# Performance work log

Measured on AMD Instinct MI355X. Metric: run time of the kernel, lower is better.

Reference implementation:

```python
import jax, jax.numpy as jnp
import numpy as np

N_NODES = 32000   # total nodes
NUM_GRAPHS = 32   # B
NODES_PER_GRAPH = 1000
N_EDGES = 256000
IN_DIM = 1024
HIDDEN = 256
C = 8             # clusters per graph


def sage_conv(x, src, dst, W_l, b_l, W_r, num_nodes):
    """PyG SAGEConv (mean aggr): out = lin_l(mean_{j in N(i)} x_j) + lin_r(x_i).
    lin_l has bias, lin_r does not. Zero in-degree -> zero aggregation."""
    msg = x[src]  # [E, F] gather from source nodes
    summed = jax.ops.segment_sum(msg, dst, num_segments=num_nodes)          # [N, F]
    cnt = jax.ops.segment_sum(jnp.ones(src.shape, x.dtype), dst, num_segments=num_nodes)  # [N]
    agg = jnp.where(cnt[:, None] > 0, summed / jnp.maximum(cnt, 1.0)[:, None], 0.0)
    return agg @ W_l + b_l + x @ W_r


def setup_inputs() -> dict:
    key = jax.random.key(0)
    ks = jax.random.split(key, 20)
    x = jax.random.normal(ks[0], (N_NODES, IN_DIM), dtype=jnp.float32)
    # edges strictly within each graph (nodes per graph contiguous)
    ge = jax.random.randint(ks[1], (N_EDGES,), 0, NUM_GRAPHS)
    sl = jax.random.randint(ks[2], (N_EDGES,), 0, NODES_PER_GRAPH)
    dl = jax.random.randint(ks[3], (N_EDGES,), 0, NODES_PER_GRAPH)
    edge_index = jnp.stack([ge * NODES_PER_GRAPH + sl, ge * NODES_PER_GRAPH + dl], axis=0)
    batch = jnp.arange(N_NODES, dtype=jnp.int32) // NODES_PER_GRAPH

    def lin(k, fi, fo):
        return jax.random.normal(k, (fi, fo), dtype=jnp.float32) / np.sqrt(fi)

    return {
        "x": x, "edge_index": edge_index, "batch": batch,
        # gnn_embed: SAGEConv(in_dim, hidden)
        "Wl1": lin(ks[4], IN_DIM, HIDDEN), "bl1": jnp.zeros((HIDDEN,), jnp.float32), "Wr1": lin(ks[5], IN_DIM, HIDDEN),
        # gnn_assign: SAGEConv(in_dim, C)
        "Wla": lin(ks[6], IN_DIM, C), "bla": jnp.zeros((C,), jnp.float32), "Wra": lin(ks[7], IN_DIM, C),
        # gnn_embed2: SAGEConv(hidden, hidden)
        "Wl2": lin(ks[8], HIDDEN, HIDDEN), "bl2": jnp.zeros((HIDDEN,), jnp.float32), "Wr2": lin(ks[9], HIDDEN, HIDDEN),
        # classifier MLP
        "Wc1": lin(ks[10], HIDDEN * C, HIDDEN), "bc1": jnp.zeros((HIDDEN,), jnp.float32),
        "Wc2": lin(ks[11], HIDDEN, 1), "bc2": jnp.zeros((1,), jnp.float32),
    }


def reference(x, edge_index, batch, Wl1, bl1, Wr1, Wla, bla, Wra, Wl2, bl2, Wr2, Wc1, bc1, Wc2, bc2):
    src, dst = edge_index[0], edge_index[1]
    n = x.shape[0]
    Z = jax.nn.relu(sage_conv(x, src, dst, Wl1, bl1, Wr1, n))   # [N, H]
    S = sage_conv(x, src, dst, Wla, bla, Wra, n)                 # [N, C]
    Ss = jax.nn.softmax(S, axis=-1)                              # row-softmax assignment
    # Per-graph DiffPool, batched via segment sums (replaces the python loop):
    # X_pool[g] = S_g^T Z_g
    Xp = jax.ops.segment_sum(Ss[:, :, None] * Z[:, None, :], batch, num_segments=NUM_GRAPHS)  # [B,C,H]
    # A_pool[g] = S_g^T A_g S_g  (A binary from to_dense_adj of within-graph edges)
    eg = batch[src]  # graph id per edge
    Ap = jax.ops.segment_sum(Ss[src][:, :, None] * Ss[dst][:, None, :], eg, num_segments=NUM_GRAPHS)  # [B,C,C]
    # dense_to_sparse(block_diag(A_pool)) drops edge weights -> binary block-diag adjacency.
    mask = (Ap != 0).astype(Z.dtype)   # edge i->j where A_pool[g,i,j] != 0
    deg = mask.sum(axis=1)             # in-degree of pooled node j: [B,C]
    agg = jnp.einsum('gij,gih->gjh', mask, Xp)  # mean over source pooled nodes
    agg = jnp.where(deg[:, :, None] > 0, agg / jnp.maximum(deg, 1.0)[:, :, None], 0.0)
    Zp = jax.nn.relu(agg @ Wl2 + bl2 + Xp @ Wr2)  # [B,C,H]
    g = Zp.reshape(NUM_GRAPHS, C * HIDDEN)
    h = jax.nn.relu(g @ Wc1 + bc1)
    return (h @ Wc2 + bc2).squeeze(-1)            # [B]
```

## Files before the change

### kernel.cpp

```cpp
#include <hip/hip_runtime.h>
#include <hip/hip_bf16.h>
#include <math.h>

#define N_NODES 32000
#define NUM_GRAPHS 32
#define NPG 1000
#define N_EDGES 256000
#define IN_DIM 1024
#define HID 256
#define NW 528
#define KBH 1040
#define WS_KS 33792
#define ZWORDS 139776

typedef _Float16 half8 __attribute__((ext_vector_type(8)));
typedef _Float16 half4 __attribute__((ext_vector_type(4)));
typedef float f32x4 __attribute__((ext_vector_type(4)));

__device__ __forceinline__ void gload16(const void* g, void* l) {
  __builtin_amdgcn_global_load_lds((const __attribute__((address_space(1))) void*)g,
                                   (__attribute__((address_space(3))) void*)l, 16, 0, 0);
}

__global__ __launch_bounds__(256) void prep_kernel(
    const float* __restrict__ Wl1, const float* __restrict__ Wr1,
    const float* __restrict__ Wla, const float* __restrict__ Wra,
    _Float16* __restrict__ WsT2, unsigned* __restrict__ zbuf)
{
  const int t = threadIdx.x;
  const int flat = blockIdx.y * 3 + blockIdx.x;
  for (int i = flat * 256 + t; i < ZWORDS; i += 384 * 256) zbuf[i] = 0u;

  const int kslot = blockIdx.y;
  const int n = blockIdx.x * 256 + t;
  if (n >= NW) return;
  const int k0 = kslot * 8;
  half8 o;
#pragma unroll
  for (int i = 0; i < 8; ++i) {
    const int k = k0 + i;
    float v;
    if (n < 256)      v = Wl1[(size_t)k * 256 + n];
    else if (n < 512) v = Wr1[(size_t)k * 256 + n - 256];
    else if (n < 520) v = Wla[(size_t)k * 8 + n - 512];
    else              v = Wra[(size_t)k * 8 + n - 520];
    o[i] = (_Float16)v;
  }
  const int ks = kslot >> 3, kb = kslot & 7;
  size_t off;
  if (n < 512) off = (size_t)ks * WS_KS + (size_t)(n >> 7) * 8192 + (kb * 128 + (n & 127)) * 8;
  else         off = (size_t)ks * WS_KS + 32768 + (kb * 16 + (n - 512)) * 8;
  *(half8*)&WsT2[off] = o;
}

__global__ __launch_bounds__(256) void xhalf_deg(
    const float* __restrict__ x, _Float16* __restrict__ XH,
    const int* __restrict__ dst, int* __restrict__ deg)
{
  const int e = blockIdx.x * 256 + threadIdx.x;
  if (e < N_EDGES) atomicAdd(&deg[dst[e]], 1);

  const size_t i = ((size_t)blockIdx.x * 256 + threadIdx.x) * 8;
  float4 a = *(const float4*)(x + i);
  float4 b = *(const float4*)(x + i + 4);
  half8 h;
  h[0] = (_Float16)a.x; h[1] = (_Float16)a.y; h[2] = (_Float16)a.z; h[3] = (_Float16)a.w;
  h[4] = (_Float16)b.x; h[5] = (_Float16)b.y; h[6] = (_Float16)b.z; h[7] = (_Float16)b.w;
  *(half8*)&XH[i] = h;
}

__global__ __launch_bounds__(256) void gemm_mfma(
    const _Float16* __restrict__ XH, const _Float16* __restrict__ WsT2,
    _Float16* __restrict__ C)
{
  const int orig = blockIdx.x;
  const int xcd = orig & 7, idx = orig >> 3;
  const int g = (xcd < 2 ? xcd * 157 : 314 + (xcd - 2) * 156) + idx;
  const int pm = g / 5, nb = g % 5;
  const int m0 = pm * 128;

  __shared__ _Float16 AH[8 * KBH];
  __shared__ _Float16 Bs[8 * KBH];

  const int tid = threadIdx.x;
  const int w = tid >> 6, l = tid & 63;
  const int wr = w >> 1, wc = w & 1;
  const int r16 = l & 15, kb4 = l >> 4;

  int lpA[4];
  const _Float16* gA[4];
#pragma unroll
  for (int j = 0; j < 4; ++j) {
    const int c = tid + j * 256;
    const int kb = c >> 7, row = c & 127;
    lpA[j] = kb * KBH + row * 8;
    gA[j] = XH + (size_t)(m0 + row) * IN_DIM + kb * 8;
  }

  if (nb < 4) {
    const _Float16* gBbase = WsT2 + nb * 8192;

    f32x4 acc[4][4] = {};
    for (int ks = 0; ks < 16; ++ks) {
      const size_t ko = (size_t)ks * 64;
      const size_t bo = (size_t)ks * WS_KS;
      __syncthreads();
#pragma unroll
      for (int j = 0; j < 4; ++j) {
        gload16(gA[j] + ko, &AH[lpA[j]]);
        gload16(gBbase + bo + (tid + j * 256) * 8, &Bs[lpA[j]]);
      }
      __syncthreads();

#pragma unroll
      for (int s = 0; s < 2; ++s) {
        const int kblk = (s * 4 + kb4) * KBH;
        half8 bf[4];
#pragma unroll
        for (int n = 0; n < 4; ++n)
          bf[n] = *(half8*)&Bs[kblk + (wc * 64 + n * 16 + r16) * 8];
#pragma unroll
        for (int m = 0; m < 4; ++m) {
          half8 ah = *(half8*)&AH[kblk + (wr * 64 + m * 16 + r16) * 8];
#pragma unroll
          for (int n = 0; n < 4; ++n)
            acc[m][n] = __builtin_amdgcn_mfma_f32_16x16x32_f16(ah, bf[n], acc[m][n], 0, 0, 0);
        }
      }
    }
    const int crow0 = m0 + wr * 64 + ((l >> 4) << 2);
    const int ccol0 = nb * 128 + wc * 64 + r16;
#pragma unroll
    for (int m = 0; m < 4; ++m)
#pragma unroll
      for (int n = 0; n < 4; ++n)
#pragma unroll
        for (int r = 0; r < 4; ++r)
          C[(size_t)(crow0 + m * 16 + r) * NW + ccol0 + n * 16] = (_Float16)acc[m][n][r];
  } else {
    f32x4 acc2[2] = {};
    for (int ks = 0; ks < 16; ++ks) {
      const size_t ko = (size_t)ks * 64;
      const size_t bo = (size_t)ks * WS_KS + 32768;
      __syncthreads();
#pragma unroll
      for (int j = 0; j < 4; ++j) gload16(gA[j] + ko, &AH[lpA[j]]);
      if (tid < 128) gload16(WsT2 + bo + tid * 8, &Bs[tid * 8]);
      __syncthreads();

#pragma unroll
      for (int s = 0; s < 2; ++s) {
        const int kb = s * 4 + kb4;
        half8 bf = *(half8*)&Bs[(kb * 16 + r16) * 8];
#pragma unroll
        for (int m = 0; m < 2; ++m) {
          half8 ah = *(half8*)&AH[kb * KBH + (w * 32 + m * 16 + r16) * 8];
          acc2[m] = __builtin_amdgcn_mfma_f32_16x16x32_f16(ah, bf, acc2[m], 0, 0, 0);
        }
      }
    }
    const int crow0 = m0 + w * 32 + ((l >> 4) << 2);
    const int ccol0 = 512 + r16;
#pragma unroll
    for (int m = 0; m < 2; ++m)
#pragma unroll
      for (int r = 0; r < 4; ++r)
        C[(size_t)(crow0 + m * 16 + r) * NW + ccol0] = (_Float16)acc2[m][r];
  }
}

__global__ __launch_bounds__(1024) void scan_kernel(const int* __restrict__ deg,
                                                    int* __restrict__ offsets) {
  __shared__ int part[1024];
  const int t = threadIdx.x;
  const int base = t * 32;
  int vals[32];
  if (t < 1000) {
#pragma unroll
    for (int j = 0; j < 8; ++j) {
      int4 v = *(const int4*)(deg + base + j * 4);
      vals[j * 4 + 0] = v.x; vals[j * 4 + 1] = v.y;
      vals[j * 4 + 2] = v.z; vals[j * 4 + 3] = v.w;
    }
  } else {
#pragma unroll
    for (int i = 0; i < 32; ++i) vals[i] = 0;
  }
  int local[32];
  int s = 0;
#pragma unroll
  for (int i = 0; i < 32; ++i) { local[i] = s; s += vals[i]; }
  part[t] = s;
  __syncthreads();
  for (int off = 1; off < 1024; off <<= 1) {
    int v = (t >= off) ? part[t - off] : 0;
    __syncthreads();
    part[t] += v;
    __syncthreads();
  }
  int excl = part[t] - s;
  if (t < 1000) {
#pragma unroll
    for (int i = 0; i < 32; ++i) offsets[base + i] = excl + local[i];
  }
  if (t == 1023) offsets[N_NODES] = part[1023];
}

__global__ void scatter_kernel(const int* __restrict__ src, const int* __restrict__ dst,
                               const int* __restrict__ offsets, int* __restrict__ cursor,
                               int* __restrict__ srcSorted) {
  int e = blockIdx.x * blockDim.x + threadIdx.x;
  if (e < N_EDGES) {
    int d = dst[e];
    int pos = offsets[d] + atomicAdd(&cursor[d], 1);
    srcSorted[pos] = src[e];
  }
}

__global__ __launch_bounds__(256) void aggregate_node(
    const _Float16* __restrict__ C,
    const int* __restrict__ offsets, const int* __restrict__ srcSorted,
    const float* __restrict__ bl1, const float* __restrict__ bla,
    _Float16* __restrict__ Zh, float* __restrict__ Ss)
{
  const int bid = blockIdx.x;
  const int wv = threadIdx.x >> 6, lane = threadIdx.x & 63;
  const int node = (bid & 7) * 4000 + (bid >> 3) * 4 + wv;
  const int b = offsets[node], e = offsets[node + 1];
  const int cnt = e - b;
  const float4 blv = *(const float4*)(bl1 + 4 * lane);
  float a0 = 0.f, a1 = 0.f, a2 = 0.f, a3 = 0.f, sp = 0.f;
  int p = b;
  int sNext = (p < e) ? srcSorted[p] : 0;
  while (p < e) {
    const int s = sNext;
    ++p;
    sNext = (p < e) ? srcSorted[p] : 0;
    const _Float16* row = C + (size_t)s * NW;
    half4 v = *(const half4*)(row + 4 * lane);
    float spv = 0.f;
    if (lane < 8) spv = (float)row[512 + lane];
    a0 += (float)v[0]; a1 += (float)v[1]; a2 += (float)v[2]; a3 += (float)v[3];
    sp += spv;
  }
  const float inv = (cnt > 0) ? 1.f / (float)cnt : 0.f;
  const _Float16* self = C + (size_t)node * NW;
  half4 sv = *(const half4*)(self + 256 + 4 * lane);
  half4 zo;
  zo[0] = (_Float16)fmaxf(a0 * inv + blv.x + (float)sv[0], 0.f);
  zo[1] = (_Float16)fmaxf(a1 * inv + blv.y + (float)sv[1], 0.f);
  zo[2] = (_Float16)fmaxf(a2 * inv + blv.z + (float)sv[2], 0.f);
  zo[3] = (_Float16)fmaxf(a3 * inv + blv.w + (float)sv[3], 0.f);
  *(half4*)(Zh + (size_t)node * 256 + 4 * lane) = zo;

  float sval = 0.f;
  if (lane < 8) sval = sp * inv + bla[lane] + (float)self[520 + lane];
  float m = sval;
  m = fmaxf(m, __shfl_xor(m, 1));
  m = fmaxf(m, __shfl_xor(m, 2));
  m = fmaxf(m, __shfl_xor(m, 4));
  float ex = expf(sval - m);
  float su = ex;
  su += __shfl_xor(su, 1);
  su += __shfl_xor(su, 2);
  su += __shfl_xor(su, 4);
  if (lane < 8) Ss[(size_t)node * 8 + lane] = ex / su;
}

__global__ __launch_bounds__(256) void pool_kernel(
    const float* __restrict__ Ss, const _Float16* __restrict__ Zh,
    const int* __restrict__ offsets, const int* __restrict__ srcSorted,
    float* __restrict__ Xp, float* __restrict__ Ap)
{
  const int g = blockIdx.x >> 3;
  const int chunk = blockIdx.x & 7;
  const int n0 = g * NPG + chunk * 125;
  const int t = threadIdx.x;
  __shared__ float lSs[125][8];
  __shared__ float lAg[125][8];
  __shared__ float apTmp[4][64];

  if (t < 125) {
    const int node = n0 + t;
    float4 s0 = *(const float4*)&Ss[(size_t)node * 8];
    float4 s1 = *(const float4*)&Ss[(size_t)node * 8 + 4];
    lSs[t][0] = s0.x; lSs[t][1] = s0.y; lSs[t][2] = s0.z; lSs[t][3] = s0.w;
    lSs[t][4] = s1.x; lSs[t][5] = s1.y; lSs[t][6] = s1.z; lSs[t][7] = s1.w;
    float a[8] = {0.f, 0.f, 0.f, 0.f, 0.f, 0.f, 0.f, 0.f};
    const int b = offsets[node], e = offsets[node + 1];
    for (int p = b; p < e; ++p) {
      const int s = srcSorted[p];
      float4 v0 = *(const float4*)&Ss[(size_t)s * 8];
      float4 v1 = *(const float4*)&Ss[(size_t)s * 8 + 4];
      a[0] += v0.x; a[1] += v0.y; a[2] += v0.z; a[3] += v0.w;
      a[4] += v1.x; a[5] += v1.y; a[6] += v1.z; a[7] += v1.w;
    }
#pragma unroll
    for (int c = 0; c < 8; ++c) lAg[t][c] = a[c];
  }
  __syncthreads();
  {
    const int sl = t >> 6, i = (t >> 3) & 7, j = t & 7;
    float acc = 0.f;
    for (int n = sl; n < 125; n += 4) acc += lAg[n][i] * lSs[n][j];
    apTmp[sl][((i << 3) | j)] = acc;
  }
  __syncthreads();
  if (t < 64) atomicAdd(&Ap[g * 64 + t], apTmp[0][t] + apTmp[1][t] + apTmp[2][t] + apTmp[3][t]);
  float xc[8] = {0.f, 0.f, 0.f, 0.f, 0.f, 0.f, 0.f, 0.f};
  for (int n = 0; n < 125; ++n) {
    float zv = (float)Zh[(size_t)(n0 + n) * 256 + t];
#pragma unroll
    for (int c = 0; c < 8; ++c) xc[c] = fmaf(lSs[n][c], zv, xc[c]);
  }
#pragma unroll
  for (int c = 0; c < 8; ++c)
    atomicAdd(&Xp[((size_t)g * 8 + c) * 256 + t], xc[c]);
}

__global__ __launch_bounds__(256) void zpcls_kernel(
    const float* __restrict__ Xp, const float* __restrict__ Ap,
    const float* __restrict__ Wl2, const float* __restrict__ bl2,
    const float* __restrict__ Wr2, const float* __restrict__ Wc1,
    float* __restrict__ Hacc)
{
  const int g = blockIdx.x >> 3;
  const int j = blockIdx.x & 7;
  const int c = threadIdx.x;
  __shared__ float lXp[8][256];
  __shared__ float agg[256];
  __shared__ float zrow[256];
  __shared__ float lAp[64];
#pragma unroll
  for (int i = 0; i < 8; ++i) lXp[i][c] = Xp[((size_t)g * 8 + i) * 256 + c];
  if (c < 64) lAp[c] = Ap[g * 64 + c];
  __syncthreads();
  {
    float d = 0.f, s = 0.f;
#pragma unroll
    for (int i = 0; i < 8; ++i) {
      bool m = (lAp[i * 8 + j] != 0.f);
      d += m ? 1.f : 0.f;
      s += m ? lXp[i][c] : 0.f;
    }
    agg[c] = (d > 0.f) ? s / fmaxf(d, 1.f) : 0.f;
  }
  __syncthreads();
  float az = bl2[c];
#pragma unroll 8
  for (int k = 0; k < 256; ++k)
    az += agg[k] * Wl2[(size_t)k * 256 + c] + lXp[j][k] * Wr2[(size_t)k * 256 + c];
  zrow[c] = fmaxf(az, 0.f);
  __syncthreads();
  float h = 0.f;
  const float* wc1 = Wc1 + (size_t)(j * 256) * 256 + c;
#pragma unroll 8
  for (int k = 0; k < 256; ++k)
    h = fmaf(zrow[k], wc1[(size_t)k * 256], h);
  atomicAdd(&Hacc[g * 256 + c], h);
}

__global__ __launch_bounds__(256) void out_kernel(
    const float* __restrict__ Hacc, const float* __restrict__ bc1,
    const float* __restrict__ Wc2, const float* __restrict__ bc2,
    float* __restrict__ out)
{
  const int g = blockIdx.x;
  const int t = threadIdx.x;
  __shared__ float red[256];
  red[t] = fmaxf(Hacc[g * 256 + t] + bc1[t], 0.f) * Wc2[t];
  __syncthreads();
  for (int off = 128; off > 0; off >>= 1) {
    if (t < off) red[t] += red[t + off];
    __syncthreads();
  }
  if (t == 0) out[g] = red[0] + bc2[0];
}

extern "C" void kernel_launch(void* const* d_in, const int* in_sizes, int n_in,
                              void* d_out, int out_size, void* d_ws, size_t ws_size,
                              hipStream_t stream) {
  const float* x   = (const float*)d_in[0];
  const int*   ei  = (const int*)d_in[1];
  const float* Wl1 = (const float*)d_in[3];
  const float* bl1 = (const float*)d_in[4];
  const float* Wr1 = (const float*)d_in[5];
  const float* Wla = (const float*)d_in[6];
  const float* bla = (const float*)d_in[7];
  const float* Wra = (const float*)d_in[8];
  const float* Wl2 = (const float*)d_in[9];
  const float* bl2 = (const float*)d_in[10];
  const float* Wr2 = (const float*)d_in[11];
  const float* Wc1 = (const float*)d_in[12];
  const float* bc1 = (const float*)d_in[13];
  const float* Wc2 = (const float*)d_in[14];
  const float* bc2 = (const float*)d_in[15];
  float* out = (float*)d_out;

  _Float16* C    = (_Float16*)d_ws;
  _Float16* WsT2 = C + (size_t)32000 * NW;
  _Float16* XH   = WsT2 + 540672;
  _Float16* Zh   = XH + (size_t)32000 * 1024;
  float* Ss   = (float*)(Zh + (size_t)32000 * 256);
  float* Xp   = Ss + 256000;
  float* Ap   = Xp + 65536;
  int* deg     = (int*)(Ap + 2048);
  int* cursor  = deg + 32000;
  float* Hacc  = (float*)(cursor + 32000);
  int* offsets = (int*)(Hacc + 8192);
  int* srcS    = offsets + 32001;
  unsigned* zbuf = (unsigned*)Xp;

  const int* src = ei;
  const int* dst = ei + N_EDGES;

  prep_kernel<<<dim3(3, 128), 256, 0, stream>>>(Wl1, Wr1, Wla, Wra, WsT2, zbuf);
  xhalf_deg<<<16000, 256, 0, stream>>>(x, XH, dst, deg);
  gemm_mfma<<<1250, 256, 0, stream>>>(XH, WsT2, C);
  scan_kernel<<<1, 1024, 0, stream>>>(deg, offsets);
  scatter_kernel<<<1000, 256, 0, stream>>>(src, dst, offsets, cursor, srcS);
  aggregate_node<<<8000, 256, 0, stream>>>(C, offsets, srcS, bl1, bla, Zh, Ss);
  pool_kernel<<<256, 256, 0, stream>>>(Ss, Zh, offsets, srcS, Xp, Ap);
  zpcls_kernel<<<256, 256, 0, stream>>>(Xp, Ap, Wl2, bl2, Wr2, Wc1, Hacc);
  out_kernel<<<32, 256, 0, stream>>>(Hacc, bc1, Wc2, bc2, out);
}
```

Before: 213.1 us.

## Double-buffer GEMM K-tiles with async LDS loads and vmcnt-based waits

Halves the GEMM K-tile to 32 and double-buffers A and B in LDS. The next-but-one tile is issued with global_load_lds while the current tile is computed, and completion is tracked with s_waitcnt vmcnt instead of full syncthreads. The weight pre-layout is changed to match the new tile size. This trades more loop iterations and barriers for overlap of global loads with MFMA work. The narrow assign-weight path is adapted to K=32 but stays single-buffered.

```diff
diff --git a/kernel.cpp b/kernel.cpp
--- a/kernel.cpp
+++ b/kernel.cpp
@@ -10,7 +10,7 @@
 #define HID 256
 #define NW 528
 #define KBH 1040
-#define WS_KS 33792
+#define WS_KS 16896
 #define ZWORDS 139776
 
 typedef _Float16 half8 __attribute__((ext_vector_type(8)));
@@ -46,10 +46,10 @@
     else              v = Wra[(size_t)k * 8 + n - 520];
     o[i] = (_Float16)v;
   }
-  const int ks = kslot >> 3, kb = kslot & 7;
+  const int K = kslot >> 2, kb = kslot & 3;
   size_t off;
-  if (n < 512) off = (size_t)ks * WS_KS + (size_t)(n >> 7) * 8192 + (kb * 128 + (n & 127)) * 8;
-  else         off = (size_t)ks * WS_KS + 32768 + (kb * 16 + (n - 512)) * 8;
+  if (n < 512) off = (size_t)K * WS_KS + (size_t)(n >> 7) * 4096 + kb * 1024 + (n & 127) * 8;
+  else         off = (size_t)K * WS_KS + 16384 + (kb * 128) + (n - 512) * 8;
   *(half8*)&WsT2[off] = o;
 }
 
@@ -79,55 +79,66 @@
   const int pm = g / 5, nb = g % 5;
   const int m0 = pm * 128;
 
-  __shared__ _Float16 AH[8 * KBH];
-  __shared__ _Float16 Bs[8 * KBH];
+  __shared__ _Float16 AH[2][4 * KBH];
+  __shared__ _Float16 Bs[2][4 * KBH];
 
   const int tid = threadIdx.x;
   const int w = tid >> 6, l = tid & 63;
   const int wr = w >> 1, wc = w & 1;
   const int r16 = l & 15, kb4 = l >> 4;
 
-  int lpA[4];
-  const _Float16* gA[4];
-#pragma unroll
-  for (int j = 0; j < 4; ++j) {
+  int lpA[2];
+  const _Float16* gA[2];
+  const _Float16* gB[2];
+#pragma unroll
+  for (int j = 0; j < 2; ++j) {
     const int c = tid + j * 256;
     const int kb = c >> 7, row = c & 127;
     lpA[j] = kb * KBH + row * 8;
     gA[j] = XH + (size_t)(m0 + row) * IN_DIM + kb * 8;
+    gB[j] = WsT2 + nb * 4096 + (size_t)c * 8;
   }
 
   if (nb < 4) {
-    const _Float16* gBbase = WsT2 + nb * 8192;
+#define STG(KS, BUF)                                             \
+    do {                                                         \
+      const size_t ko_ = (size_t)(KS) * 32;                      \
+      const size_t bo_ = (size_t)(KS) * WS_KS;                   \
+      gload16(gA[0] + ko_, &AH[BUF][lpA[0]]);                    \
+      gload16(gA[1] + ko_, &AH[BUF][lpA[1]]);                    \
+      gload16(gB[0] + bo_, &Bs[BUF][lpA[0]]);                    \
+      gload16(gB[1] + bo_, &Bs[BUF][lpA[1]]);                    \
+    } while (0)
 
     f32x4 acc[4][4] = {};
-    for (int ks = 0; ks < 16; ++ks) {
-      const size_t ko = (size_t)ks * 64;
-      const size_t bo = (size_t)ks * WS_KS;
-      __syncthreads();
-#pragma unroll
-      for (int j = 0; j < 4; ++j) {
-        gload16(gA[j] + ko, &AH[lpA[j]]);
-        gload16(gBbase + bo + (tid + j * 256) * 8, &Bs[lpA[j]]);
+    STG(0, 0);
+    STG(1, 1);
+    for (int ks = 0; ks < 32; ++ks) {
+      const int cur = ks & 1;
+      if (ks < 31) asm volatile("s_waitcnt vmcnt(4)" ::: "memory");
+      else         asm volatile("s_waitcnt vmcnt(0)" ::: "memory");
+      __builtin_amdgcn_s_barrier();
+      __builtin_amdgcn_sched_barrier(0);
+
+      half8 bf[4];
+#pragma unroll
+      for (int n = 0; n < 4; ++n)
+        bf[n] = *(half8*)&Bs[cur][kb4 * KBH + (wc * 64 + n * 16 + r16) * 8];
+#pragma unroll
+      for (int m = 0; m < 4; ++m) {
+        half8 ah = *(half8*)&AH[cur][kb4 * KBH + (wr * 64 + m * 16 + r16) * 8];
+#pragma unroll
+        for (int n = 0; n < 4; ++n)
+          acc[m][n] = __builtin_amdgcn_mfma_f32_16x16x32_f16(ah, bf[n], acc[m][n], 0, 0, 0);
       }
-      __syncthreads();
-
-#pragma unroll
-      for (int s = 0; s < 2; ++s) {
-        const int kblk = (s * 4 + kb4) * KBH;
-        half8 bf[4];
-#pragma unroll
-        for (int n = 0; n < 4; ++n)
-          bf[n] = *(half8*)&Bs[kblk + (wc * 64 + n * 16 + r16) * 8];
-#pragma unroll
-        for (int m = 0; m < 4; ++m) {
-          half8 ah = *(half8*)&AH[kblk + (wr * 64 + m * 16 + r16) * 8];
-#pragma unroll
-          for (int n = 0; n < 4; ++n)
-            acc[m][n] = __builtin_amdgcn_mfma_f32_16x16x32_f16(ah, bf[n], acc[m][n], 0, 0, 0);
-        }
-      }
+
+      __builtin_amdgcn_sched_barrier(0);
+      asm volatile("" ::: "memory");
+      __builtin_amdgcn_s_barrier();
+      if (ks + 2 < 32) STG(ks + 2, cur);
     }
+#undef STG
+
     const int crow0 = m0 + wr * 64 + ((l >> 4) << 2);
     const int ccol0 = nb * 128 + wc * 64 + r16;
 #pragma unroll
@@ -139,24 +150,20 @@
           C[(size_t)(crow0 + m * 16 + r) * NW + ccol0 + n * 16] = (_Float16)acc[m][n][r];
   } else {
     f32x4 acc2[2] = {};
-    for (int ks = 0; ks < 16; ++ks) {
-      const size_t ko = (size_t)ks * 64;
-      const size_t bo = (size_t)ks * WS_KS + 32768;
+    for (int ks = 0; ks < 32; ++ks) {
+      const size_t ko = (size_t)ks * 32;
+      const size_t bo = (size_t)ks * WS_KS + 16384;
       __syncthreads();
-#pragma unroll
-      for (int j = 0; j < 4; ++j) gload16(gA[j] + ko, &AH[lpA[j]]);
-      if (tid < 128) gload16(WsT2 + bo + tid * 8, &Bs[tid * 8]);
+      gload16(gA[0] + ko, &AH[0][lpA[0]]);
+      gload16(gA[1] + ko, &AH[0][lpA[1]]);
+      if (tid < 64) gload16(WsT2 + bo + tid * 8, &Bs[0][tid * 8]);
       __syncthreads();
 
-#pragma unroll
-      for (int s = 0; s < 2; ++s) {
-        const int kb = s * 4 + kb4;
-        half8 bf = *(half8*)&Bs[(kb * 16 + r16) * 8];
-#pragma unroll
-        for (int m = 0; m < 2; ++m) {
-          half8 ah = *(half8*)&AH[kb * KBH + (w * 32 + m * 16 + r16) * 8];
-          acc2[m] = __builtin_amdgcn_mfma_f32_16x16x32_f16(ah, bf, acc2[m], 0, 0, 0);
-        }
+      half8 bf = *(half8*)&Bs[0][(kb4 * 16 + r16) * 8];
+#pragma unroll
+      for (int m = 0; m < 2; ++m) {
+        half8 ah = *(half8*)&AH[0][kb4 * KBH + (w * 32 + m * 16 + r16) * 8];
+        acc2[m] = __builtin_amdgcn_mfma_f32_16x16x32_f16(ah, bf, acc2[m], 0, 0, 0);
       }
     }
     const int crow0 = m0 + w * 32 + ((l >> 4) << 2);
```

Measured after the change: 214.6 us. Within noise of the previous version (+0.7%).
